# Performance work log

Measured on AMD Instinct MI355X. Metric: run time of the kernel, lower is better.

The kernel has to match this reference:

```python
import jax, jax.numpy as jnp
import numpy as np

DIM = 512
HEADS = 8
HEAD_DIM = DIM // HEADS
MLP_HIDDEN = int(DIM * 4.0)
B, N = 4, 2048
LS_INIT = 1e-5
EPS = 1e-5


def _layernorm(x, w, b):
    mu = jnp.mean(x, axis=-1, keepdims=True)
    var = jnp.mean(jnp.square(x - mu), axis=-1, keepdims=True)
    return (x - mu) * jax.lax.rsqrt(var + EPS) * w + b


def setup_inputs() -> dict:
    key = jax.random.key(0)
    ks = jax.random.split(key, 12)
    s = 0.02
    return {
        "x": jax.random.normal(ks[0], (B, N, DIM), jnp.float32),
        "rel_pos_bias": jax.random.normal(ks[1], (HEADS, N, N), jnp.float32),
        "qkv_w": jax.random.normal(ks[2], (DIM, 3 * DIM), jnp.float32) * s,
        "qkv_b": jnp.zeros((3 * DIM,), jnp.float32),
        "out_w": jax.random.normal(ks[3], (DIM, DIM), jnp.float32) * s,
        "out_b": jnp.zeros((DIM,), jnp.float32),
        "ln1_w": jnp.ones((DIM,), jnp.float32),
        "ln1_b": jnp.zeros((DIM,), jnp.float32),
        "ln2_w": jnp.ones((DIM,), jnp.float32),
        "ln2_b": jnp.zeros((DIM,), jnp.float32),
        "ffn_w1": jax.random.normal(ks[4], (DIM, MLP_HIDDEN), jnp.float32) * s,
        "ffn_b1": jnp.zeros((MLP_HIDDEN,), jnp.float32),
        "ffn_w2": jax.random.normal(ks[5], (MLP_HIDDEN, DIM), jnp.float32) * s,
        "ffn_b2": jnp.zeros((DIM,), jnp.float32),
        "gamma1": jnp.full((DIM,), LS_INIT, jnp.float32),
        "gamma2": jnp.full((DIM,), LS_INIT, jnp.float32),
    }


def reference(x, rel_pos_bias, qkv_w, qkv_b, out_w, out_b, ln1_w, ln1_b,
              ln2_w, ln2_b, ffn_w1, ffn_b1, ffn_w2, ffn_b2, gamma1, gamma2):
    # Pre-norm MHA with relative-position bias
    y = _layernorm(x, ln1_w, ln1_b)                       # [B,N,C]
    qkv = y @ qkv_w + qkv_b                               # [B,N,3C]
    qkv = qkv.reshape(B, N, 3, HEADS, HEAD_DIM)
    q = jnp.transpose(qkv[:, :, 0], (0, 2, 1, 3))         # [B,H,N,D]
    k = jnp.transpose(qkv[:, :, 1], (0, 2, 1, 3))
    v = jnp.transpose(qkv[:, :, 2], (0, 2, 1, 3))
    scale = 1.0 / np.sqrt(HEAD_DIM).astype(np.float32)
    attn = jnp.einsum("bhid,bhjd->bhij", q, k) * scale    # [B,H,N,N]
    attn = attn + rel_pos_bias[None]
    attn = jax.nn.softmax(attn, axis=-1)
    out = jnp.einsum("bhij,bhjd->bhid", attn, v)          # [B,H,N,D]
    out = jnp.transpose(out, (0, 2, 1, 3)).reshape(B, N, DIM)
    out = out @ out_w + out_b
    x = x + out * gamma1                                  # layer scale, no drop-path (eval)
    # FFN with exact GELU
    y2 = _layernorm(x, ln2_w, ln2_b)
    h = jax.nn.gelu(y2 @ ffn_w1 + ffn_b1, approximate=False)
    ffn_out = h @ ffn_w2 + ffn_b2
    x = x + ffn_out * gamma2
    return x
```

## Files before the change

kernel.cpp:

```cpp
#include <hip/hip_runtime.h>
#include <hip/hip_bf16.h>
#include <math.h>

#define SEQ 2048
#define BATCH 4
#define DM 512
#define NH 8
#define HD 64
#define HID 2048
#define ROWS (BATCH * SEQ)

typedef __attribute__((ext_vector_type(8))) short short8;
typedef __attribute__((ext_vector_type(4))) float f32x4;

__device__ __forceinline__ short f2bf(float f) {
    unsigned u = __float_as_uint(f);
    u += 0x7fff + ((u >> 16) & 1);
    return (short)(u >> 16);
}

__device__ __forceinline__ void gl2lds16(const void* g, void* l) {
    __builtin_amdgcn_global_load_lds(
        (const __attribute__((address_space(1))) void*)g,
        (__attribute__((address_space(3))) void*)l, 16, 0, 0);
}

__global__ __launch_bounds__(256) void tcast_all(
    const float* __restrict__ qkv_w, const float* __restrict__ out_w,
    const float* __restrict__ w1, const float* __restrict__ w2,
    short* __restrict__ o_qkv, short* __restrict__ o_out,
    short* __restrict__ o_w1, short* __restrict__ o_w2) {
    __shared__ float tile[32][33];
    int id = blockIdx.x;
    const float* W; short* O; int K, N;
    if (id < 768)       { W = qkv_w; O = o_qkv; K = 512;  N = 1536; }
    else if (id < 1024) { W = out_w; O = o_out; K = 512;  N = 512;  id -= 768; }
    else if (id < 2048) { W = w1;    O = o_w1;  K = 512;  N = 2048; id -= 1024; }
    else                { W = w2;    O = o_w2;  K = 2048; N = 512;  id -= 2048; }
    int tn = N / 32;
    int n0 = (id % tn) * 32, k0 = (id / tn) * 32;
    int tx = threadIdx.x, ty = threadIdx.y;
#pragma unroll
    for (int i = 0; i < 4; ++i)
        tile[ty + i * 8][tx] = W[(size_t)(k0 + ty + i * 8) * N + n0 + tx];
    __syncthreads();
#pragma unroll
    for (int i = 0; i < 4; ++i)
        O[(size_t)(n0 + ty + i * 8) * K + k0 + tx] = f2bf(tile[tx][ty + i * 8]);
}

__global__ __launch_bounds__(256) void ln_k(const float* __restrict__ X,
                                            const float* __restrict__ g,
                                            const float* __restrict__ bta,
                                            short* __restrict__ Y) {
    int t = threadIdx.x;
    int wv = t >> 6, ln = t & 63;
    size_t row = (size_t)blockIdx.x * 4 + wv;
    const float* xr = X + row * DM;
    float4 v0 = *(const float4*)(xr + ln * 4);
    float4 v1 = *(const float4*)(xr + 256 + ln * 4);
    float s = v0.x + v0.y + v0.z + v0.w + v1.x + v1.y + v1.z + v1.w;
    float q = v0.x * v0.x + v0.y * v0.y + v0.z * v0.z + v0.w * v0.w +
              v1.x * v1.x + v1.y * v1.y + v1.z * v1.z + v1.w * v1.w;
#pragma unroll
    for (int off = 1; off < 64; off <<= 1) {
        s += __shfl_xor(s, off);
        q += __shfl_xor(q, off);
    }
    float mean = s * (1.0f / 512.0f);
    float var = q * (1.0f / 512.0f) - mean * mean;
    float rstd = rsqrtf(var + 1e-5f);
    int c0 = ln * 4, c1 = 256 + ln * 4;
    ushort4 o0, o1;
    o0.x = (unsigned short)f2bf((v0.x - mean) * rstd * g[c0 + 0] + bta[c0 + 0]);
    o0.y = (unsigned short)f2bf((v0.y - mean) * rstd * g[c0 + 1] + bta[c0 + 1]);
    o0.z = (unsigned short)f2bf((v0.z - mean) * rstd * g[c0 + 2] + bta[c0 + 2]);
    o0.w = (unsigned short)f2bf((v0.w - mean) * rstd * g[c0 + 3] + bta[c0 + 3]);
    o1.x = (unsigned short)f2bf((v1.x - mean) * rstd * g[c1 + 0] + bta[c1 + 0]);
    o1.y = (unsigned short)f2bf((v1.y - mean) * rstd * g[c1 + 1] + bta[c1 + 1]);
    o1.z = (unsigned short)f2bf((v1.z - mean) * rstd * g[c1 + 2] + bta[c1 + 2]);
    o1.w = (unsigned short)f2bf((v1.w - mean) * rstd * g[c1 + 3] + bta[c1 + 3]);
    *(ushort4*)((unsigned short*)Y + row * DM + c0) = o0;
    *(ushort4*)((unsigned short*)Y + row * DM + c1) = o1;
}

template <int EPI, int TN, int BM>
__global__ __launch_bounds__(256) void gemm_bt(const short* __restrict__ A,
                                               const short* __restrict__ Bt,
                                               const float* __restrict__ bias,
                                               const float* __restrict__ gamma,
                                               const float* __restrict__ res,
                                               void* __restrict__ Cout,
                                               int M, int N, int K, int gx) {
    constexpr int NI = TN / 32;
    constexpr int MI = BM / 32;
    __shared__ __attribute__((aligned(16))) short As[2][2][BM][32];
    __shared__ __attribute__((aligned(16))) short Bs[2][2][TN][32];
    int t = threadIdx.x;
    int w = t >> 6, ln = t & 63;
    int quad = ln >> 4, l15 = ln & 15;
    int nwg = gridDim.x;
    int qq = nwg >> 3;
    int sw = ((blockIdx.x & 7) * qq) + (blockIdx.x >> 3);
    int bx = sw % gx, by = sw / gx;
    int n0 = bx * TN, m0 = by * BM;
    int wm = (w & 1) * (BM / 2), wn = (w >> 1) * (TN / 2);

    int srow0 = w * 32 + (ln >> 2);
    int srow1 = srow0 + 16;
    int srowH = w * 16 + (ln >> 2);
    int schunk = (ln & 3) * 8;
    const short* Ag0 = A + (size_t)(m0 + srow0) * K + schunk;
    const short* Ag1 = A + (size_t)(m0 + srow1) * K + schunk;
    const short* AgH = A + (size_t)(m0 + srowH) * K + schunk;
    const short* Bg0 = Bt + (size_t)(n0 + srow0) * K + schunk;
    const short* Bg1 = Bt + (size_t)(n0 + srow1) * K + schunk;
    const short* BgH = Bt + (size_t)(n0 + srowH) * K + schunk;

    f32x4 acc[MI][NI];
#pragma unroll
    for (int i = 0; i < MI; ++i)
#pragma unroll
        for (int j = 0; j < NI; ++j) acc[i][j] = (f32x4){0.f, 0.f, 0.f, 0.f};

    auto STAGE = [&](int buf, int k0) {
        if constexpr (BM == 128) {
            gl2lds16(Ag0 + k0, &As[buf][0][srow0][schunk]);
            gl2lds16(Ag1 + k0, &As[buf][0][srow1][schunk]);
            gl2lds16(Ag0 + k0 + 32, &As[buf][1][srow0][schunk]);
            gl2lds16(Ag1 + k0 + 32, &As[buf][1][srow1][schunk]);
        } else {
            gl2lds16(AgH + k0, &As[buf][0][srowH][schunk]);
            gl2lds16(AgH + k0 + 32, &As[buf][1][srowH][schunk]);
        }
        if constexpr (TN == 128) {
            gl2lds16(Bg0 + k0, &Bs[buf][0][srow0 & 127][schunk]);
            gl2lds16(Bg1 + k0, &Bs[buf][0][srow1 & 127][schunk]);
            gl2lds16(Bg0 + k0 + 32, &Bs[buf][1][srow0 & 127][schunk]);
            gl2lds16(Bg1 + k0 + 32, &Bs[buf][1][srow1 & 127][schunk]);
        } else {
            gl2lds16(BgH + k0, &Bs[buf][0][srowH & (TN - 1)][schunk]);
            gl2lds16(BgH + k0 + 32, &Bs[buf][1][srowH & (TN - 1)][schunk]);
        }
    };

    STAGE(0, 0);
    __syncthreads();

    int NS = K >> 6;
    for (int s = 0; s < NS; ++s) {
        int cur = s & 1;
        if (s + 1 < NS) STAGE(cur ^ 1, (s + 1) << 6);
#pragma unroll
        for (int hh = 0; hh < 2; ++hh) {
            short8 af[MI], bf[NI];
#pragma unroll
            for (int mi = 0; mi < MI; ++mi)
                af[mi] = *(const short8*)&As[cur][hh][wm + mi * 16 + l15][quad * 8];
#pragma unroll
            for (int ni = 0; ni < NI; ++ni)
                bf[ni] = *(const short8*)&Bs[cur][hh][wn + ni * 16 + l15][quad * 8];
#pragma unroll
            for (int mi = 0; mi < MI; ++mi)
#pragma unroll
                for (int ni = 0; ni < NI; ++ni)
                    acc[mi][ni] = __builtin_amdgcn_mfma_f32_16x16x32_bf16(
                        af[mi], bf[ni], acc[mi][ni], 0, 0, 0);
        }
        __syncthreads();
    }

#pragma unroll
    for (int mi = 0; mi < MI; ++mi) {
#pragma unroll
        for (int ni = 0; ni < NI; ++ni) {
#pragma unroll
            for (int r = 0; r < 4; ++r) {
                int row = m0 + wm + mi * 16 + quad * 4 + r;
                int col = n0 + wn + ni * 16 + l15;
                float v = acc[mi][ni][r] + bias[col];
                if (EPI == 0) {
                    ((short*)Cout)[(size_t)row * N + col] = f2bf(v);
                } else if (EPI == 1) {
                    float u = v * fmaf(v * v, 0.0713548162f, 1.59576912f);
                    float gg = v / (1.0f + __expf(-u));
                    ((short*)Cout)[(size_t)row * N + col] = f2bf(gg);
                } else {
                    ((float*)Cout)[(size_t)row * N + col] =
                        fmaf(v, gamma[col], res[(size_t)row * N + col]);
                }
            }
        }
    }
}

__global__ __launch_bounds__(256) void qkvbias_k(
    const short* __restrict__ A, const short* __restrict__ Bt,
    const float* __restrict__ qkvb, short* __restrict__ Cout,
    short* __restrict__ Cout2,
    const float* __restrict__ bias, short* __restrict__ biasP) {
    __shared__ __attribute__((aligned(16))) char smem[33024];
    int bid = blockIdx.x;
    int grp = bid / 11, sub = bid % 11;
    int t = threadIdx.x;
    int w = t >> 6, ln = t & 63;
    int quad = ln >> 4, l15 = ln & 15;

    if (sub < 3) {
        typedef short (*tile32)[32];
        tile32 As0 = (tile32)smem;
        tile32 As1 = (tile32)(smem + 8192);
        tile32 Bs0 = (tile32)(smem + 16384);
        tile32 Bs1 = (tile32)(smem + 24576);
        const int K = 512, N = 1536;
        int g = grp * 3 + sub;
        int n0 = (g % 12) * 128, m0 = (g / 12) * 128;
        int wm = (w & 1) * 64, wn = (w >> 1) * 64;

        int srow0 = w * 32 + (ln >> 2);
        int srow1 = srow0 + 16;
        int schunk = (ln & 3) * 8;
        const short* Ag0 = A + (size_t)(m0 + srow0) * K + schunk;
        const short* Ag1 = A + (size_t)(m0 + srow1) * K + schunk;
        const short* Bg0 = Bt + (size_t)(n0 + srow0) * K + schunk;
        const short* Bg1 = Bt + (size_t)(n0 + srow1) * K + schunk;

        f32x4 acc[4][4];
#pragma unroll
        for (int i = 0; i < 4; ++i)
#pragma unroll
            for (int j = 0; j < 4; ++j) acc[i][j] = (f32x4){0.f, 0.f, 0.f, 0.f};

        for (int k0 = 0; k0 < K; k0 += 64) {
            __syncthreads();
            gl2lds16(Ag0 + k0, &As0[srow0][schunk]);
            gl2lds16(Ag1 + k0, &As0[srow1][schunk]);
            gl2lds16(Ag0 + k0 + 32, &As1[srow0][schunk]);
            gl2lds16(Ag1 + k0 + 32, &As1[srow1][schunk]);
            gl2lds16(Bg0 + k0, &Bs0[srow0][schunk]);
            gl2lds16(Bg1 + k0, &Bs0[srow1][schunk]);
            gl2lds16(Bg0 + k0 + 32, &Bs1[srow0][schunk]);
            gl2lds16(Bg1 + k0 + 32, &Bs1[srow1][schunk]);
            __syncthreads();
            {
                short8 af[4], bf[4];
#pragma unroll
                for (int mi = 0; mi < 4; ++mi)
                    af[mi] = *(const short8*)&As0[wm + mi * 16 + l15][quad * 8];
#pragma unroll
                for (int ni = 0; ni < 4; ++ni)
                    bf[ni] = *(const short8*)&Bs0[wn + ni * 16 + l15][quad * 8];
#pragma unroll
                for (int mi = 0; mi < 4; ++mi)
#pragma unroll
                    for (int ni = 0; ni < 4; ++ni)
                        acc[mi][ni] = __builtin_amdgcn_mfma_f32_16x16x32_bf16(
                            af[mi], bf[ni], acc[mi][ni], 0, 0, 0);
            }
            {
                short8 af[4], bf[4];
#pragma unroll
                for (int mi = 0; mi < 4; ++mi)
                    af[mi] = *(const short8*)&As1[wm + mi * 16 + l15][quad * 8];
#pragma unroll
                for (int ni = 0; ni < 4; ++ni)
                    bf[ni] = *(const short8*)&Bs1[wn + ni * 16 + l15][quad * 8];
#pragma unroll
                for (int mi = 0; mi < 4; ++mi)
#pragma unroll
                    for (int ni = 0; ni < 4; ++ni)
                        acc[mi][ni] = __builtin_amdgcn_mfma_f32_16x16x32_bf16(
                            af[mi], bf[ni], acc[mi][ni], 0, 0, 0);
            }
        }

        if (n0 >= 1024) {
#pragma unroll
            for (int mi = 0; mi < 4; ++mi) {
#pragma unroll
                for (int ni = 0; ni < 4; ++ni) {
                    int col = n0 + wn + ni * 16 + l15;
                    int d = col - 1024, hh = d >> 6, dd = d & 63;
                    int row0 = m0 + wm + mi * 16 + quad * 4;
                    int bb = row0 >> 11, key = row0 & 2047;
                    float bs = qkvb[col];
                    ushort4 pk;
                    pk.x = (unsigned short)f2bf(acc[mi][ni][0] + bs);
                    pk.y = (unsigned short)f2bf(acc[mi][ni][1] + bs);
                    pk.z = (unsigned short)f2bf(acc[mi][ni][2] + bs);
                    pk.w = (unsigned short)f2bf(acc[mi][ni][3] + bs);
                    *(ushort4*)&Cout2[((size_t)(bb * 8 + hh) * 64 + dd) * 2048 + key] = pk;
                }
            }
        } else {
#pragma unroll
            for (int mi = 0; mi < 4; ++mi) {
#pragma unroll
                for (int ni = 0; ni < 4; ++ni) {
#pragma unroll
                    for (int r = 0; r < 4; ++r) {
                        int row = m0 + wm + mi * 16 + quad * 4 + r;
                        int col = n0 + wn + ni * 16 + l15;
                        float v = acc[mi][ni][r] + qkvb[col];
                        float sc = (n0 < 512) ? 0.18033688f : 1.0f;
                        Cout[(size_t)row * 1024 + col] = f2bf(v * sc);
                    }
                }
            }
        }
    } else {
        typedef short (*tile1032)[1032];
        tile1032 tl = (tile1032)smem;
        int id = grp * 8 + (sub - 3);
        int half = id & 1;
        int g = (id >> 1) & 127;
        int h = id >> 8;
        const float* src = bias + (size_t)h * SEQ * SEQ + (size_t)g * 16 * SEQ + half * 1024;
#pragma unroll
        for (int i = 0; i < 16; ++i) {
            float4 v = *(const float4*)(src + (size_t)i * SEQ + t * 4);
            float2 lo, hi;
            lo.x = v.x * 1.44269504f; lo.y = v.y * 1.44269504f;
            hi.x = v.z * 1.44269504f; hi.y = v.w * 1.44269504f;
            __hip_bfloat162 l2 = __float22bfloat162_rn(lo);
            __hip_bfloat162 h2 = __float22bfloat162_rn(hi);
            uint2 pp;
            pp.x = *(unsigned*)&l2;
            pp.y = *(unsigned*)&h2;
            *(uint2*)&tl[i][t * 4] = pp;
        }
        __syncthreads();
        int jtbase = half * 16;
#pragma unroll
        for (int u = 0; u < 4; ++u) {
            int jl = w * 4 + u;
            int tau = (h * 128 + g) * 32 + jtbase + jl;
#pragma unroll
            for (int n2 = 0; n2 < 2; ++n2) {
                uint2 a = *(const uint2*)&tl[l15][jl * 64 + n2 * 32 + quad * 4];
                uint2 b = *(const uint2*)&tl[l15][jl * 64 + n2 * 32 + 16 + quad * 4];
                uint4 pp;
                pp.x = a.x; pp.y = a.y; pp.z = b.x; pp.w = b.y;
                *(uint4*)(biasP + (size_t)tau * 1024 + n2 * 512 + ln * 8) = pp;
            }
        }
    }
}

__global__ __launch_bounds__(256, 3) void attn_k(const short* __restrict__ qkv,
                                                 const short* __restrict__ vT,
                                                 const short* __restrict__ biasP,
                                                 short* __restrict__ Aout) {
    __shared__ __attribute__((aligned(16))) short Ks[2][64 * 64];
    __shared__ __attribute__((aligned(16))) short Vs[2][64 * 64];
    __shared__ __attribute__((aligned(16))) short Ps[4][2][16 * 64];
    int t = threadIdx.x;
    int w = t >> 6, ln = t & 63, quad = ln >> 4, l15 = ln & 15;
    int idx = blockIdx.x;
    int h = idx & 7, b = (idx >> 3) & 3, qt = idx >> 5;
    int qb = qt * 128 + w * 16;
    const size_t cbase = (size_t)b * SEQ * 1024;

    const short* qrow0 = qkv + cbase + (size_t)(qb + l15) * 1024 + h * 64;
    const short* qrow1 = qrow0 + (size_t)64 * 1024;
    short8 qf[2][2];
    qf[0][0] = *(const short8*)(qrow0 + quad * 8);
    qf[0][1] = *(const short8*)(qrow0 + 32 + quad * 8);
    qf[1][0] = *(const short8*)(qrow1 + quad * 8);
    qf[1][1] = *(const short8*)(qrow1 + 32 + quad * 8);

    int kr = t >> 3, kc = t & 7;
    int sc = (kc ^ (kr & 7)) * 8;
    const short* kgS = qkv + cbase + 512 + h * 64 + sc;
    const short* vgS = vT + (size_t)(b * 8 + h) * 64 * 2048 + sc;

    int g0 = qt * 8 + w;
    const short* bp0 = biasP + ((size_t)(h * 128 + g0) * 32) * 1024 + ln * 8;
    const short* bp1 = biasP + ((size_t)(h * 128 + g0 + 4) * 32) * 1024 + ln * 8;

    short8 ones;
#pragma unroll
    for (int i = 0; i < 8; ++i) ones[i] = (short)0x3F80;

    f32x4 o[2][4], ol[2];
#pragma unroll
    for (int qg = 0; qg < 2; ++qg) {
#pragma unroll
        for (int db = 0; db < 4; ++db) o[qg][db] = (f32x4){0.f, 0.f, 0.f, 0.f};
        ol[qg] = (f32x4){0.f, 0.f, 0.f, 0.f};
    }

    int sw7 = l15 & 7;

    gl2lds16(kgS,                              &Ks[0][t * 8]);
    gl2lds16(kgS + (size_t)32 * 1024,          &Ks[0][2048 + t * 8]);
    gl2lds16(vgS,                              &Vs[0][t * 8]);
    gl2lds16(vgS + (size_t)32 * 2048,          &Vs[0][2048 + t * 8]);
    uint4 bbc[2][2];
#pragma unroll
    for (int n2 = 0; n2 < 2; ++n2) {
        bbc[0][n2] = *(const uint4*)(bp0 + n2 * 512);
        bbc[1][n2] = *(const uint4*)(bp1 + n2 * 512);
    }

    int cur = 0;
    for (int jt = 0; jt < 32; ++jt) {
        __syncthreads();
        int jn = (jt < 31) ? (jt + 1) : jt;
        int j1 = jn * 64;
        int nxt = cur ^ 1;
        gl2lds16(kgS + (size_t)(j1 + kr) * 1024,      &Ks[nxt][t * 8]);
        gl2lds16(kgS + (size_t)(j1 + 32 + kr) * 1024, &Ks[nxt][2048 + t * 8]);
        gl2lds16(vgS + (size_t)kr * 2048 + j1,        &Vs[nxt][t * 8]);
        gl2lds16(vgS + (size_t)(32 + kr) * 2048 + j1, &Vs[nxt][2048 + t * 8]);

        f32x4 s4[2][4];
        __builtin_amdgcn_s_setprio(1);
#pragma unroll
        for (int ni = 0; ni < 4; ++ni) {
            short8 k0 = *(const short8*)&Ks[cur][(ni * 16 + l15) * 64 + ((quad ^ sw7) * 8)];
            short8 k1 = *(const short8*)&Ks[cur][(ni * 16 + l15) * 64 + (((4 + quad) ^ sw7) * 8)];
#pragma unroll
            for (int qg = 0; qg < 2; ++qg) {
                uint4 bb = bbc[qg][ni >> 1];
                unsigned lo = (ni & 1) ? bb.z : bb.x;
                unsigned hi = (ni & 1) ? bb.w : bb.y;
                f32x4 z;
                z[0] = __uint_as_float(lo << 16);
                z[1] = __uint_as_float(lo & 0xffff0000u);
                z[2] = __uint_as_float(hi << 16);
                z[3] = __uint_as_float(hi & 0xffff0000u);
                z = __builtin_amdgcn_mfma_f32_16x16x32_bf16(k0, qf[qg][0], z, 0, 0, 0);
                s4[qg][ni] = __builtin_amdgcn_mfma_f32_16x16x32_bf16(k1, qf[qg][1], z, 0, 0, 0);
            }
        }
        __builtin_amdgcn_s_setprio(0);
#pragma unroll
        for (int n2 = 0; n2 < 2; ++n2) {
            bbc[0][n2] = *(const uint4*)(bp0 + (size_t)jn * 1024 + n2 * 512);
            bbc[1][n2] = *(const uint4*)(bp1 + (size_t)jn * 1024 + n2 * 512);
        }
#pragma unroll
        for (int qg = 0; qg < 2; ++qg) {
#pragma unroll
            for (int ni = 0; ni < 4; ++ni) {
                float2 plo, phi;
                plo.x = exp2f(s4[qg][ni][0]);
                plo.y = exp2f(s4[qg][ni][1]);
                phi.x = exp2f(s4[qg][ni][2]);
                phi.y = exp2f(s4[qg][ni][3]);
                __hip_bfloat162 l2 = __float22bfloat162_rn(plo);
                __hip_bfloat162 h2 = __float22bfloat162_rn(phi);
                union { uint2 u; } pp;
                pp.u.x = *(unsigned*)&l2;
                pp.u.y = *(unsigned*)&h2;
                int c = ni * 2 + (quad >> 1);
                *(uint2*)&Ps[w][qg][l15 * 64 + ((c ^ sw7) * 8) + (quad & 1) * 4] = pp.u;
            }
        }
        __builtin_amdgcn_s_setprio(1);
#pragma unroll
        for (int kk = 0; kk < 2; ++kk) {
            short8 ap0 = *(const short8*)&Ps[w][0][l15 * 64 + (((kk * 4 + quad) ^ sw7) * 8)];
            short8 ap1 = *(const short8*)&Ps[w][1][l15 * 64 + (((kk * 4 + quad) ^ sw7) * 8)];
#pragma unroll
            for (int db = 0; db < 4; ++db) {
                short8 vv = *(const short8*)&Vs[cur][(db * 16 + l15) * 64 + (((kk * 4 + quad) ^ sw7) * 8)];
                o[0][db] = __builtin_amdgcn_mfma_f32_16x16x32_bf16(ap0, vv, o[0][db], 0, 0, 0);
                o[1][db] = __builtin_amdgcn_mfma_f32_16x16x32_bf16(ap1, vv, o[1][db], 0, 0, 0);
            }
            ol[0] = __builtin_amdgcn_mfma_f32_16x16x32_bf16(ap0, ones, ol[0], 0, 0, 0);
            ol[1] = __builtin_amdgcn_mfma_f32_16x16x32_bf16(ap1, ones, ol[1], 0, 0, 0);
        }
        __builtin_amdgcn_s_setprio(0);
        cur = nxt;
    }
#pragma unroll
    for (int qg = 0; qg < 2; ++qg) {
#pragma unroll
        for (int r = 0; r < 4; ++r) {
            float inv = 1.0f / ol[qg][r];
            int qrow_g = b * SEQ + qb + qg * 64 + quad * 4 + r;
#pragma unroll
            for (int db = 0; db < 4; ++db) {
                Aout[(size_t)qrow_g * DM + h * 64 + db * 16 + l15] =
                    f2bf(o[qg][db][r] * inv);
            }
        }
    }
}

extern "C" void kernel_launch(void* const* d_in, const int* in_sizes, int n_in,
                              void* d_out, int out_size, void* d_ws, size_t ws_size,
                              hipStream_t stream) {
    const float* x      = (const float*)d_in[0];
    const float* bias   = (const float*)d_in[1];
    const float* qkv_w  = (const float*)d_in[2];
    const float* qkv_b  = (const float*)d_in[3];
    const float* out_w  = (const float*)d_in[4];
    const float* out_b  = (const float*)d_in[5];
    const float* ln1_w  = (const float*)d_in[6];
    const float* ln1_b  = (const float*)d_in[7];
    const float* ln2_w  = (const float*)d_in[8];
    const float* ln2_b  = (const float*)d_in[9];
    const float* ffn_w1 = (const float*)d_in[10];
    const float* ffn_b1 = (const float*)d_in[11];
    const float* ffn_w2 = (const float*)d_in[12];
    const float* ffn_b2 = (const float*)d_in[13];
    const float* gamma1 = (const float*)d_in[14];
    const float* gamma2 = (const float*)d_in[15];
    float* out = (float*)d_out;

    short* wqkvT = (short*)d_ws;
    short* woutT = wqkvT + (size_t)1536 * 512;
    short* w1T   = woutT + (size_t)512 * 512;
    short* w2T   = w1T + (size_t)2048 * 512;
    short* y1    = w2T + (size_t)512 * 2048;
    short* qkvB  = y1 + (size_t)ROWS * DM;
    short* vTb   = qkvB + (size_t)ROWS * 1024;
    short* aoutB = vTb + (size_t)32 * 64 * 2048;
    float* x1    = (float*)(aoutB + (size_t)ROWS * DM);
    short* biasPw = (short*)(x1 + (size_t)ROWS * DM);
    short* hB    = qkvB;

    tcast_all<<<3072, dim3(32, 8), 0, stream>>>(qkv_w, out_w, ffn_w1, ffn_w2,
                                                wqkvT, woutT, w1T, w2T);
    ln_k<<<ROWS / 4, 256, 0, stream>>>(x, ln1_w, ln1_b, y1);
    qkvbias_k<<<2816, 256, 0, stream>>>(y1, wqkvT, qkv_b, qkvB, vTb,
                                        bias, biasPw);
    attn_k<<<512, 256, 0, stream>>>(qkvB, vTb, biasPw, aoutB);
    gemm_bt<2, 128, 64><<<512, 256, 0, stream>>>(
        aoutB, woutT, out_b, gamma1, x, x1, ROWS, 512, 512, 4);
    ln_k<<<ROWS / 4, 256, 0, stream>>>(x1, ln2_w, ln2_b, y1);
    gemm_bt<1, 128, 128><<<1024, 256, 0, stream>>>(
        y1, w1T, ffn_b1, nullptr, nullptr, hB, ROWS, 2048, 512, 16);
    gemm_bt<2, 128, 64><<<512, 256, 0, stream>>>(
        hB, w2T, ffn_b2, gamma2, x1, out, ROWS, 512, 2048, 4);
}
```

Measured before the change: 418.4 us.

## Merge weight casts and LayerNorm into fewer launches, overlap casts with QKV

The qkv weight transpose-cast and the first LayerNorm now run in one kernel, with blocks interleaved across the grid. The transpose-casts of the other three weights move into the QKV/bias-permute kernel as extra block types, since they are not needed until later GEMMs. This removes two kernel launches and lets the independent cast work fill idle CUs next to the GEMM and bias-permute blocks. The block-index mapping now depends on exact grid arithmetic (groups of 11 and 20), and the larger heterogeneous grid may unbalance scheduling.

```diff
diff --git a/kernel.cpp b/kernel.cpp
--- a/kernel.cpp
+++ b/kernel.cpp
@@ -25,28 +25,58 @@
         (__attribute__((address_space(3))) void*)l, 16, 0, 0);
 }
 
-__global__ __launch_bounds__(256) void tcast_all(
-    const float* __restrict__ qkv_w, const float* __restrict__ out_w,
-    const float* __restrict__ w1, const float* __restrict__ w2,
-    short* __restrict__ o_qkv, short* __restrict__ o_out,
-    short* __restrict__ o_w1, short* __restrict__ o_w2) {
+__global__ __launch_bounds__(256) void pre1_k(
+    const float* __restrict__ qkv_w, short* __restrict__ o_qkv,
+    const float* __restrict__ X, const float* __restrict__ lg,
+    const float* __restrict__ lb, short* __restrict__ Y) {
     __shared__ float tile[32][33];
-    int id = blockIdx.x;
-    const float* W; short* O; int K, N;
-    if (id < 768)       { W = qkv_w; O = o_qkv; K = 512;  N = 1536; }
-    else if (id < 1024) { W = out_w; O = o_out; K = 512;  N = 512;  id -= 768; }
-    else if (id < 2048) { W = w1;    O = o_w1;  K = 512;  N = 2048; id -= 1024; }
-    else                { W = w2;    O = o_w2;  K = 2048; N = 512;  id -= 2048; }
-    int tn = N / 32;
-    int n0 = (id % tn) * 32, k0 = (id / tn) * 32;
-    int tx = threadIdx.x, ty = threadIdx.y;
-#pragma unroll
-    for (int i = 0; i < 4; ++i)
-        tile[ty + i * 8][tx] = W[(size_t)(k0 + ty + i * 8) * N + n0 + tx];
-    __syncthreads();
-#pragma unroll
-    for (int i = 0; i < 4; ++i)
-        O[(size_t)(n0 + ty + i * 8) * K + k0 + tx] = f2bf(tile[tx][ty + i * 8]);
+    int bid = blockIdx.x;
+    int grp = bid / 11, sub = bid % 11;
+    int t = threadIdx.x;
+    if (sub < 3) {
+        int id = grp * 3 + sub;
+        const int K = 512, N = 1536;
+        int tn = N / 32;
+        int n0 = (id % tn) * 32, k0 = (id / tn) * 32;
+        int tx = t & 31, ty = t >> 5;
+#pragma unroll
+        for (int i = 0; i < 4; ++i)
+            tile[ty + i * 8][tx] = qkv_w[(size_t)(k0 + ty + i * 8) * N + n0 + tx];
+        __syncthreads();
+#pragma unroll
+        for (int i = 0; i < 4; ++i)
+            o_qkv[(size_t)(n0 + ty + i * 8) * K + k0 + tx] = f2bf(tile[tx][ty + i * 8]);
+    } else {
+        int lbk = grp * 8 + (sub - 3);
+        int wv = t >> 6, ln = t & 63;
+        size_t row = (size_t)lbk * 4 + wv;
+        const float* xr = X + row * DM;
+        float4 v0 = *(const float4*)(xr + ln * 4);
+        float4 v1 = *(const float4*)(xr + 256 + ln * 4);
+        float s = v0.x + v0.y + v0.z + v0.w + v1.x + v1.y + v1.z + v1.w;
+        float q = v0.x * v0.x + v0.y * v0.y + v0.z * v0.z + v0.w * v0.w +
+                  v1.x * v1.x + v1.y * v1.y + v1.z * v1.z + v1.w * v1.w;
+#pragma unroll
+        for (int off = 1; off < 64; off <<= 1) {
+            s += __shfl_xor(s, off);
+            q += __shfl_xor(q, off);
+        }
+        float mean = s * (1.0f / 512.0f);
+        float var = q * (1.0f / 512.0f) - mean * mean;
+        float rstd = rsqrtf(var + 1e-5f);
+        int c0 = ln * 4, c1 = 256 + ln * 4;
+        ushort4 o0, o1;
+        o0.x = (unsigned short)f2bf((v0.x - mean) * rstd * lg[c0 + 0] + lb[c0 + 0]);
+        o0.y = (unsigned short)f2bf((v0.y - mean) * rstd * lg[c0 + 1] + lb[c0 + 1]);
+        o0.z = (unsigned short)f2bf((v0.z - mean) * rstd * lg[c0 + 2] + lb[c0 + 2]);
+        o0.w = (unsigned short)f2bf((v0.w - mean) * rstd * lg[c0 + 3] + lb[c0 + 3]);
+        o1.x = (unsigned short)f2bf((v1.x - mean) * rstd * lg[c1 + 0] + lb[c1 + 0]);
+        o1.y = (unsigned short)f2bf((v1.y - mean) * rstd * lg[c1 + 1] + lb[c1 + 1]);
+        o1.z = (unsigned short)f2bf((v1.z - mean) * rstd * lg[c1 + 2] + lb[c1 + 2]);
+        o1.w = (unsigned short)f2bf((v1.w - mean) * rstd * lg[c1 + 3] + lb[c1 + 3]);
+        *(ushort4*)((unsigned short*)Y + row * DM + c0) = o0;
+        *(ushort4*)((unsigned short*)Y + row * DM + c1) = o1;
+    }
 }
 
 __global__ __launch_bounds__(256) void ln_k(const float* __restrict__ X,
@@ -198,10 +228,13 @@
     const short* __restrict__ A, const short* __restrict__ Bt,
     const float* __restrict__ qkvb, short* __restrict__ Cout,
     short* __restrict__ Cout2,
-    const float* __restrict__ bias, short* __restrict__ biasP) {
+    const float* __restrict__ bias, short* __restrict__ biasP,
+    const float* __restrict__ out_w, const float* __restrict__ w1,
+    const float* __restrict__ w2, short* __restrict__ o_out,
+    short* __restrict__ o_w1, short* __restrict__ o_w2) {
     __shared__ __attribute__((aligned(16))) char smem[33024];
     int bid = blockIdx.x;
-    int grp = bid / 11, sub = bid % 11;
+    int grp = bid / 20, sub = bid % 20;
     int t = threadIdx.x;
     int w = t >> 6, ln = t & 63;
     int quad = ln >> 4, l15 = ln & 15;
@@ -308,7 +341,7 @@
                 }
             }
         }
-    } else {
+    } else if (sub < 11) {
         typedef short (*tile1032)[1032];
         tile1032 tl = (tile1032)smem;
         int id = grp * 8 + (sub - 3);
@@ -344,6 +377,23 @@
                 *(uint4*)(biasP + (size_t)tau * 1024 + n2 * 512 + ln * 8) = pp;
             }
         }
+    } else {
+        float (*tile)[33] = (float(*)[33])smem;
+        int id = 768 + grp * 9 + (sub - 11);
+        const float* W; short* O; int K, N;
+        if (id < 1024)      { W = out_w; O = o_out; K = 512;  N = 512;  id -= 768; }
+        else if (id < 2048) { W = w1;    O = o_w1;  K = 512;  N = 2048; id -= 1024; }
+        else                { W = w2;    O = o_w2;  K = 2048; N = 512;  id -= 2048; }
+        int tn = N / 32;
+        int n0 = (id % tn) * 32, k0 = (id / tn) * 32;
+        int tx = t & 31, ty = t >> 5;
+#pragma unroll
+        for (int i = 0; i < 4; ++i)
+            tile[ty + i * 8][tx] = W[(size_t)(k0 + ty + i * 8) * N + n0 + tx];
+        __syncthreads();
+#pragma unroll
+        for (int i = 0; i < 4; ++i)
+            O[(size_t)(n0 + ty + i * 8) * K + k0 + tx] = f2bf(tile[tx][ty + i * 8]);
     }
 }
 
@@ -523,11 +573,11 @@
     short* biasPw = (short*)(x1 + (size_t)ROWS * DM);
     short* hB    = qkvB;
 
-    tcast_all<<<3072, dim3(32, 8), 0, stream>>>(qkv_w, out_w, ffn_w1, ffn_w2,
-                                                wqkvT, woutT, w1T, w2T);
-    ln_k<<<ROWS / 4, 256, 0, stream>>>(x, ln1_w, ln1_b, y1);
-    qkvbias_k<<<2816, 256, 0, stream>>>(y1, wqkvT, qkv_b, qkvB, vTb,
-                                        bias, biasPw);
+    pre1_k<<<2816, 256, 0, stream>>>(qkv_w, wqkvT, x, ln1_w, ln1_b, y1);
+    qkvbias_k<<<5120, 256, 0, stream>>>(y1, wqkvT, qkv_b, qkvB, vTb,
+                                        bias, biasPw,
+                                        out_w, ffn_w1, ffn_w2,
+                                        woutT, w1T, w2T);
     attn_k<<<512, 256, 0, stream>>>(qkvB, vTb, biasPw, aoutB);
     gemm_bt<2, 128, 64><<<512, 256, 0, stream>>>(
         aoutB, woutT, out_b, gamma1, x, x1, ROWS, 512, 512, 4);
```

Result: no change. 423.0 us (+1.1%).
